# Kernel tuning notes

Hardware: AMD Instinct MI355X
Metric: run time of the kernel (lower is better)

## Reference

```python
import jax, jax.numpy as jnp
import numpy as np
from functools import reduce

N_QUBITS = 12          # input_shape[-2] = 2**12 = 4096; must be multiple of 4
DIM = 2 ** N_QUBITS
N_GATES = N_QUBITS // 4  # one diamond U-gate (4 qubits, 16x16) per group
BATCH = 128
TWO_PI = 6.283185307179586


def setup_inputs() -> dict:
    key = jax.random.key(0)
    k1, k2, k3, k4 = jax.random.split(key, 4)
    thetas = jax.random.uniform(k1, (N_GATES,), jnp.float32, 0.0, TWO_PI)
    # Fixed Hermitian generator for the 16x16 gate, pre-diagonalized:
    # U(theta) = V @ diag(exp(-i*theta*evals)) @ V^T
    rng = np.random.RandomState(42)
    H = rng.randn(16, 16).astype(np.float32)
    H = (H + H.T) * 0.5
    evals_np, evecs_np = np.linalg.eigh(H)
    evecs = jnp.asarray(evecs_np, jnp.float32)
    evals = jnp.asarray(evals_np, jnp.float32)
    state_real = jax.random.normal(k3, (BATCH, DIM, 1), jnp.float32)
    state_imag = jax.random.normal(k4, (BATCH, DIM, 1), jnp.float32)
    return {"thetas": thetas, "evecs": evecs, "evals": evals,
            "state_real": state_real, "state_imag": state_imag}


def _gate(theta, evecs, evals):
    # 16x16 unitary: V diag(exp(-i theta lambda)) V^T  (V real orthogonal)
    phase = jnp.exp(-1j * (theta * evals).astype(jnp.complex64))  # [16]
    V = evecs.astype(jnp.complex64)
    return (V * phase[None, :]) @ V.T  # [16,16] complex64


def reference(thetas, evecs, evals, state_real, state_imag):
    # Build each 4-qubit gate, then the full unitary via Kronecker product
    Us = [_gate(thetas[i], evecs, evals) for i in range(N_GATES)]
    U_full = reduce(jnp.kron, Us)  # [DIM, DIM] complex64 (the anti-pattern)
    psi = state_real.astype(jnp.complex64) + 1j * state_imag.astype(jnp.complex64)
    out = jnp.einsum('ij,bjk->bik', U_full, psi)  # U @ inputs
    # stack real/imag so output is a single real array: [2, BATCH, DIM, 1]
    return jnp.stack([jnp.real(out), jnp.imag(out)])
```

## Files before the change

kernel.cpp:

```cpp
#include <hip/hip_runtime.h>

#define DIM 4096
#define NB 128
#define S1 17
#define S0 274

__global__ __launch_bounds__(256)
void ulayer_kernel(const float* __restrict__ thetas,
                   const float* __restrict__ evecs,
                   const float* __restrict__ evals,
                   const float* __restrict__ sre,
                   const float* __restrict__ sim,
                   float* __restrict__ out)
{
    __shared__ float  sV[256];
    __shared__ float  sC[48];
    __shared__ float  sS[48];
    __shared__ float2 sG[3][16][16];
    __shared__ float2 st[16 * S0];

    const int t = threadIdx.x;
    const int b = blockIdx.x;

    sV[t] = evecs[t];
    if (t < 48) {
        const int g = t >> 4, k = t & 15;
        const float a = thetas[g] * evals[k];
        float sn, cs;
        sincosf(a, &sn, &cs);
        sC[t] = cs;
        sS[t] = sn;
    }

    const float4* __restrict__ vre = (const float4*)(sre + (size_t)b * DIM);
    const float4* __restrict__ vim = (const float4*)(sim + (size_t)b * DIM);
    float4 lre[4], lim[4];
#pragma unroll
    for (int it = 0; it < 4; ++it) {
        lre[it] = vre[t + 256 * it];
        lim[it] = vim[t + 256 * it];
    }

    __syncthreads();

#pragma unroll
    for (int rep = 0; rep < 3; ++rep) {
        const int e = t + (rep << 8);
        const int g = e >> 8;
        const int i = (e >> 4) & 15;
        const int j = e & 15;
        float gr = 0.f, gi = 0.f;
#pragma unroll
        for (int k = 0; k < 16; ++k) {
            const float vv = sV[i * 16 + k] * sV[j * 16 + k];
            gr = fmaf(vv,  sC[(g << 4) + k], gr);
            gi = fmaf(vv, -sS[(g << 4) + k], gi);
        }
        sG[g][i][j] = make_float2(gr, gi);
    }

#pragma unroll
    for (int it = 0; it < 4; ++it) {
        const int e0 = (t + 256 * it) << 2;
        const int i0 = e0 >> 8;
        const int r  = e0 & 255;
        const int base = i0 * S0 + (r >> 4) * S1 + (r & 15);
        const float* pr = (const float*)&lre[it];
        const float* pi = (const float*)&lim[it];
#pragma unroll
        for (int q = 0; q < 4; ++q)
            st[base + q] = make_float2(pr[q], pi[q]);
    }
    __syncthreads();

    const int h = t >> 4;
    const int k = t & 15;

    auto pass = [&](const int gidx, const int base, const int stride) {
        float2 x[16];
#pragma unroll
        for (int j = 0; j < 16; ++j) x[j] = st[base + j * stride];
        float2 y[16];
#pragma unroll
        for (int i = 0; i < 16; ++i) {
            float ar = 0.f, ai = 0.f;
#pragma unroll
            for (int j = 0; j < 16; ++j) {
                const float2 g = sG[gidx][i][j];
                ar = fmaf(g.x,  x[j].x, ar);
                ar = fmaf(-g.y, x[j].y, ar);
                ai = fmaf(g.x,  x[j].y, ai);
                ai = fmaf(g.y,  x[j].x, ai);
            }
            y[i] = make_float2(ar, ai);
        }
#pragma unroll
        for (int i = 0; i < 16; ++i) st[base + i * stride] = y[i];
    };

    pass(2, h * S0 + k * S1, 1);
    __syncthreads();
    pass(1, h * S0 + k, S1);
    __syncthreads();
    pass(0, h * S1 + k, S0);
    __syncthreads();

    float* __restrict__ ore = out + (size_t)b * DIM;
    float* __restrict__ oim = out + (size_t)NB * DIM + (size_t)b * DIM;
#pragma unroll
    for (int it = 0; it < 4; ++it) {
        const int e0 = (t + 256 * it) << 2;
        const int i0 = e0 >> 8;
        const int r  = e0 & 255;
        const int base = i0 * S0 + (r >> 4) * S1 + (r & 15);
        float4 xr, xi;
        float* qr = (float*)&xr;
        float* qi = (float*)&xi;
#pragma unroll
        for (int q = 0; q < 4; ++q) {
            const float2 v = st[base + q];
            qr[q] = v.x;
            qi[q] = v.y;
        }
        *(float4*)(ore + e0) = xr;
        *(float4*)(oim + e0) = xi;
    }
}

extern "C" void kernel_launch(void* const* d_in, const int* in_sizes, int n_in,
                              void* d_out, int out_size, void* d_ws, size_t ws_size,
                              hipStream_t stream) {
    const float* thetas = (const float*)d_in[0];
    const float* evecs  = (const float*)d_in[1];
    const float* evals  = (const float*)d_in[2];
    const float* sre    = (const float*)d_in[3];
    const float* sim    = (const float*)d_in[4];
    float* out = (float*)d_out;
    ulayer_kernel<<<NB, 256, 0, stream>>>(thetas, evecs, evals, sre, sim, out);
}
```

Baseline: 78.91 us.

## Double threads per block and split gate rows across threads in each pass

Moves the block from 256 to 512 threads. Each thread now keeps two gate rows in registers and handles four fibers, where it previously handled one full 16-row fiber. Because a fiber's outputs are now written by several threads, each pass gets an extra barrier between reading inputs and writing results. The aim is more waves per CU to hide LDS latency while keeping per-thread register use in check, at the cost of reading each fiber's inputs 8x redundantly from LDS and adding barriers.

After: 70.16 us. 11.1% less time.

```diff
diff --git a/kernel.cpp b/kernel.cpp
--- a/kernel.cpp
+++ b/kernel.cpp
@@ -2,10 +2,11 @@
 
 #define DIM 4096
 #define NB 128
+#define NT 512
 #define S1 17
 #define S0 274
 
-__global__ __launch_bounds__(256)
+__global__ __launch_bounds__(NT)
 void ulayer_kernel(const float* __restrict__ thetas,
                    const float* __restrict__ evecs,
                    const float* __restrict__ evals,
@@ -22,46 +23,48 @@
     const int t = threadIdx.x;
     const int b = blockIdx.x;
 
-    sV[t] = evecs[t];
-    if (t < 48) {
-        const int g = t >> 4, k = t & 15;
-        const float a = thetas[g] * evals[k];
+    if (t < 256) sV[t] = evecs[t];
+    else if (t < 304) {
+        const int e = t - 256;
+        const int g = e >> 4, k = e & 15;
         float sn, cs;
-        sincosf(a, &sn, &cs);
-        sC[t] = cs;
-        sS[t] = sn;
+        sincosf(thetas[g] * evals[k], &sn, &cs);
+        sC[e] = cs;
+        sS[e] = sn;
     }
 
     const float4* __restrict__ vre = (const float4*)(sre + (size_t)b * DIM);
     const float4* __restrict__ vim = (const float4*)(sim + (size_t)b * DIM);
-    float4 lre[4], lim[4];
+    float4 lre[2], lim[2];
 #pragma unroll
-    for (int it = 0; it < 4; ++it) {
-        lre[it] = vre[t + 256 * it];
-        lim[it] = vim[t + 256 * it];
+    for (int it = 0; it < 2; ++it) {
+        lre[it] = vre[t + NT * it];
+        lim[it] = vim[t + NT * it];
     }
 
     __syncthreads();
 
 #pragma unroll
-    for (int rep = 0; rep < 3; ++rep) {
-        const int e = t + (rep << 8);
-        const int g = e >> 8;
-        const int i = (e >> 4) & 15;
-        const int j = e & 15;
-        float gr = 0.f, gi = 0.f;
+    for (int rep = 0; rep < 2; ++rep) {
+        const int e = t + (rep << 9);
+        if (e < 768) {
+            const int g = e >> 8;
+            const int i = (e >> 4) & 15;
+            const int j = e & 15;
+            float gr = 0.f, gi = 0.f;
 #pragma unroll
-        for (int k = 0; k < 16; ++k) {
-            const float vv = sV[i * 16 + k] * sV[j * 16 + k];
-            gr = fmaf(vv,  sC[(g << 4) + k], gr);
-            gi = fmaf(vv, -sS[(g << 4) + k], gi);
+            for (int k = 0; k < 16; ++k) {
+                const float vv = sV[i * 16 + k] * sV[j * 16 + k];
+                gr = fmaf(vv,  sC[(g << 4) + k], gr);
+                gi = fmaf(vv, -sS[(g << 4) + k], gi);
+            }
+            sG[g][i][j] = make_float2(gr, gi);
         }
-        sG[g][i][j] = make_float2(gr, gi);
     }
 
 #pragma unroll
-    for (int it = 0; it < 4; ++it) {
-        const int e0 = (t + 256 * it) << 2;
+    for (int it = 0; it < 2; ++it) {
+        const int e0 = (t + NT * it) << 2;
         const int i0 = e0 >> 8;
         const int r  = e0 & 255;
         const int base = i0 * S0 + (r >> 4) * S1 + (r & 15);
@@ -73,43 +76,64 @@
     }
     __syncthreads();
 
-    const int h = t >> 4;
-    const int k = t & 15;
+    const int fg = t & 63;
+    const int ih = t >> 6;
+    const int r0 = ih * 2;
 
-    auto pass = [&](const int gidx, const int base, const int stride) {
-        float2 x[16];
+    auto pass = [&](const int gidx, const int BH, const int BK, const int STRIDE) {
+        float2 g0[16], g1[16];
 #pragma unroll
-        for (int j = 0; j < 16; ++j) x[j] = st[base + j * stride];
-        float2 y[16];
+        for (int j = 0; j < 16; ++j) {
+            g0[j] = sG[gidx][r0][j];
+            g1[j] = sG[gidx][r0 + 1][j];
+        }
+        float2 y0[4], y1[4];
 #pragma unroll
-        for (int i = 0; i < 16; ++i) {
-            float ar = 0.f, ai = 0.f;
+        for (int fl = 0; fl < 4; ++fl) {
+            const int f = fg + 64 * fl;
+            const int h = f >> 4;
+            const int k = f & 15;
+            const int base = h * BH + k * BK;
+            float2 x[16];
+#pragma unroll
+            for (int j = 0; j < 16; ++j) x[j] = st[base + j * STRIDE];
+            float ar0 = 0.f, ai0 = 0.f, ar1 = 0.f, ai1 = 0.f;
 #pragma unroll
             for (int j = 0; j < 16; ++j) {
-                const float2 g = sG[gidx][i][j];
-                ar = fmaf(g.x,  x[j].x, ar);
-                ar = fmaf(-g.y, x[j].y, ar);
-                ai = fmaf(g.x,  x[j].y, ai);
-                ai = fmaf(g.y,  x[j].x, ai);
+                ar0 = fmaf(g0[j].x,  x[j].x, ar0);
+                ar0 = fmaf(-g0[j].y, x[j].y, ar0);
+                ai0 = fmaf(g0[j].x,  x[j].y, ai0);
+                ai0 = fmaf(g0[j].y,  x[j].x, ai0);
+                ar1 = fmaf(g1[j].x,  x[j].x, ar1);
+                ar1 = fmaf(-g1[j].y, x[j].y, ar1);
+                ai1 = fmaf(g1[j].x,  x[j].y, ai1);
+                ai1 = fmaf(g1[j].y,  x[j].x, ai1);
             }
-            y[i] = make_float2(ar, ai);
+            y0[fl] = make_float2(ar0, ai0);
+            y1[fl] = make_float2(ar1, ai1);
         }
+        __syncthreads();
 #pragma unroll
-        for (int i = 0; i < 16; ++i) st[base + i * stride] = y[i];
+        for (int fl = 0; fl < 4; ++fl) {
+            const int f = fg + 64 * fl;
+            const int h = f >> 4;
+            const int k = f & 15;
+            const int base = h * BH + k * BK;
+            st[base + r0 * STRIDE]       = y0[fl];
+            st[base + (r0 + 1) * STRIDE] = y1[fl];
+        }
+        __syncthreads();
     };
 
-    pass(2, h * S0 + k * S1, 1);
-    __syncthreads();
-    pass(1, h * S0 + k, S1);
-    __syncthreads();
-    pass(0, h * S1 + k, S0);
-    __syncthreads();
+    pass(2, S0, S1, 1);
+    pass(1, S0, 1, S1);
+    pass(0, S1, 1, S0);
 
     float* __restrict__ ore = out + (size_t)b * DIM;
     float* __restrict__ oim = out + (size_t)NB * DIM + (size_t)b * DIM;
 #pragma unroll
-    for (int it = 0; it < 4; ++it) {
-        const int e0 = (t + 256 * it) << 2;
+    for (int it = 0; it < 2; ++it) {
+        const int e0 = (t + NT * it) << 2;
         const int i0 = e0 >> 8;
         const int r  = e0 & 255;
         const int base = i0 * S0 + (r >> 4) * S1 + (r & 15);
@@ -136,5 +160,5 @@
     const float* sre    = (const float*)d_in[3];
     const float* sim    = (const float*)d_in[4];
     float* out = (float*)d_out;
-    ulayer_kernel<<<NB, 256, 0, stream>>>(thetas, evecs, evals, sre, sim, out);
+    ulayer_kernel<<<NB, NT, 0, stream>>>(thetas, evecs, evals, sre, sim, out);
 }
```

## Split contraction into two kernels with four blocks per batch row

Applied to the files above, without the earlier changes.

Replaces the single 128-block kernel with two kernels of 512 blocks each. The first applies gates 2 and 1 on quarter-slices of each state and writes the intermediate complex state to workspace. The second applies gate 0 across the remaining axis. The contraction pass is also restructured so each thread holds two gate rows in registers rather than reading the gate from shared memory. This targets low occupancy, since only 128 blocks were spread over the GPU, at the cost of an extra launch, a global round trip for the intermediate state, and recomputing the gates in every block.

Result: faster. 73.70 us (-6.6%).

```diff
diff --git a/kernel.cpp b/kernel.cpp
--- a/kernel.cpp
+++ b/kernel.cpp
@@ -1,52 +1,95 @@
 #include <hip/hip_runtime.h>
 
 #define DIM 4096
-#define NB 128
-#define S1 17
-#define S0 274
+#define BATCH 128
+#define K1S0 274
+#define K1S1 17
+#define K2S0 69
+#define K2S1 17
+
+__device__ __forceinline__ void contract_pass(float2* __restrict__ st,
+                                              const float2 (*__restrict__ G)[16],
+                                              const int t, const int BH,
+                                              const int BK, const int STRIDE)
+{
+    const int fpair = t & 31;
+    const int r0 = (t >> 5) << 1;
+    float2 g0[16], g1[16];
+#pragma unroll
+    for (int j = 0; j < 16; ++j) {
+        g0[j] = G[r0][j];
+        g1[j] = G[r0 + 1][j];
+    }
+    float2 y[2][2];
+#pragma unroll
+    for (int fl = 0; fl < 2; ++fl) {
+        const int f = fpair + (fl << 5);
+        const int base = (f >> 4) * BH + (f & 15) * BK;
+        float2 x[16];
+#pragma unroll
+        for (int j = 0; j < 16; ++j) x[j] = st[base + j * STRIDE];
+        float ar0 = 0.f, ai0 = 0.f, ar1 = 0.f, ai1 = 0.f;
+#pragma unroll
+        for (int j = 0; j < 16; ++j) {
+            ar0 = fmaf(g0[j].x,  x[j].x, ar0);
+            ar0 = fmaf(-g0[j].y, x[j].y, ar0);
+            ai0 = fmaf(g0[j].x,  x[j].y, ai0);
+            ai0 = fmaf(g0[j].y,  x[j].x, ai0);
+            ar1 = fmaf(g1[j].x,  x[j].x, ar1);
+            ar1 = fmaf(-g1[j].y, x[j].y, ar1);
+            ai1 = fmaf(g1[j].x,  x[j].y, ai1);
+            ai1 = fmaf(g1[j].y,  x[j].x, ai1);
+        }
+        y[fl][0] = make_float2(ar0, ai0);
+        y[fl][1] = make_float2(ar1, ai1);
+    }
+    __syncthreads();
+#pragma unroll
+    for (int fl = 0; fl < 2; ++fl) {
+        const int f = fpair + (fl << 5);
+        const int base = (f >> 4) * BH + (f & 15) * BK;
+        st[base + r0 * STRIDE]       = y[fl][0];
+        st[base + (r0 + 1) * STRIDE] = y[fl][1];
+    }
+    __syncthreads();
+}
 
 __global__ __launch_bounds__(256)
-void ulayer_kernel(const float* __restrict__ thetas,
-                   const float* __restrict__ evecs,
-                   const float* __restrict__ evals,
-                   const float* __restrict__ sre,
-                   const float* __restrict__ sim,
-                   float* __restrict__ out)
+void ulayer_k1(const float* __restrict__ thetas,
+               const float* __restrict__ evecs,
+               const float* __restrict__ evals,
+               const float* __restrict__ sre,
+               const float* __restrict__ sim,
+               float2* __restrict__ ws)
 {
     __shared__ float  sV[256];
     __shared__ float  sC[48];
     __shared__ float  sS[48];
     __shared__ float2 sG[3][16][16];
-    __shared__ float2 st[16 * S0];
+    __shared__ float2 st[4 * K1S0];
 
     const int t = threadIdx.x;
-    const int b = blockIdx.x;
+    const int b = blockIdx.x >> 2;
+    const int q = blockIdx.x & 3;
 
     sV[t] = evecs[t];
     if (t < 48) {
         const int g = t >> 4, k = t & 15;
-        const float a = thetas[g] * evals[k];
         float sn, cs;
-        sincosf(a, &sn, &cs);
+        sincosf(thetas[g] * evals[k], &sn, &cs);
         sC[t] = cs;
         sS[t] = sn;
     }
 
-    const float4* __restrict__ vre = (const float4*)(sre + (size_t)b * DIM);
-    const float4* __restrict__ vim = (const float4*)(sim + (size_t)b * DIM);
-    float4 lre[4], lim[4];
-#pragma unroll
-    for (int it = 0; it < 4; ++it) {
-        lre[it] = vre[t + 256 * it];
-        lim[it] = vim[t + 256 * it];
-    }
-
-    __syncthreads();
-
-#pragma unroll
-    for (int rep = 0; rep < 3; ++rep) {
+    const float4 re4 = *(const float4*)(sre + (size_t)b * DIM + q * 1024 + t * 4);
+    const float4 im4 = *(const float4*)(sim + (size_t)b * DIM + q * 1024 + t * 4);
+
+    __syncthreads();
+
+#pragma unroll
+    for (int rep = 0; rep < 2; ++rep) {
         const int e = t + (rep << 8);
-        const int g = e >> 8;
+        const int g = 1 + (e >> 8);
         const int i = (e >> 4) & 15;
         const int j = e & 15;
         float gr = 0.f, gi = 0.f;
@@ -59,72 +102,93 @@
         sG[g][i][j] = make_float2(gr, gi);
     }
 
-#pragma unroll
-    for (int it = 0; it < 4; ++it) {
-        const int e0 = (t + 256 * it) << 2;
-        const int i0 = e0 >> 8;
-        const int r  = e0 & 255;
-        const int base = i0 * S0 + (r >> 4) * S1 + (r & 15);
-        const float* pr = (const float*)&lre[it];
-        const float* pi = (const float*)&lim[it];
-#pragma unroll
-        for (int q = 0; q < 4; ++q)
-            st[base + q] = make_float2(pr[q], pi[q]);
-    }
-    __syncthreads();
-
-    const int h = t >> 4;
-    const int k = t & 15;
-
-    auto pass = [&](const int gidx, const int base, const int stride) {
-        float2 x[16];
-#pragma unroll
-        for (int j = 0; j < 16; ++j) x[j] = st[base + j * stride];
-        float2 y[16];
-#pragma unroll
-        for (int i = 0; i < 16; ++i) {
-            float ar = 0.f, ai = 0.f;
-#pragma unroll
-            for (int j = 0; j < 16; ++j) {
-                const float2 g = sG[gidx][i][j];
-                ar = fmaf(g.x,  x[j].x, ar);
-                ar = fmaf(-g.y, x[j].y, ar);
-                ai = fmaf(g.x,  x[j].y, ai);
-                ai = fmaf(g.y,  x[j].x, ai);
-            }
-            y[i] = make_float2(ar, ai);
+    const int e0  = t << 2;
+    const int li0 = e0 >> 8;
+    const int i1  = (e0 >> 4) & 15;
+    const int i2  = e0 & 15;
+    const int sbase = li0 * K1S0 + i1 * K1S1 + i2;
+    st[sbase + 0] = make_float2(re4.x, im4.x);
+    st[sbase + 1] = make_float2(re4.y, im4.y);
+    st[sbase + 2] = make_float2(re4.z, im4.z);
+    st[sbase + 3] = make_float2(re4.w, im4.w);
+    __syncthreads();
+
+    contract_pass(st, sG[2], t, K1S0, K1S1, 1);
+    contract_pass(st, sG[1], t, K1S0, 1, K1S1);
+
+    const float2 a0 = st[sbase + 0];
+    const float2 a1 = st[sbase + 1];
+    const float2 a2 = st[sbase + 2];
+    const float2 a3 = st[sbase + 3];
+    float4* wp = (float4*)(ws + (size_t)b * DIM + q * 1024 + e0);
+    wp[0] = make_float4(a0.x, a0.y, a1.x, a1.y);
+    wp[1] = make_float4(a2.x, a2.y, a3.x, a3.y);
+}
+
+__global__ __launch_bounds__(256)
+void ulayer_k2(const float* __restrict__ thetas,
+               const float* __restrict__ evecs,
+               const float* __restrict__ evals,
+               const float2* __restrict__ ws,
+               float* __restrict__ out)
+{
+    __shared__ float  sV[256];
+    __shared__ float  sC[16];
+    __shared__ float  sS[16];
+    __shared__ float2 sG0[16][16];
+    __shared__ float2 st[16 * K2S0];
+
+    const int t = threadIdx.x;
+    const int b = blockIdx.x >> 2;
+    const int p = blockIdx.x & 3;
+
+    sV[t] = evecs[t];
+    if (t < 16) {
+        float sn, cs;
+        sincosf(thetas[0] * evals[t], &sn, &cs);
+        sC[t] = cs;
+        sS[t] = sn;
+    }
+
+    const int i0 = t >> 4;
+    const int r0 = (t & 15) << 2;
+    const float2* wrow = ws + (size_t)b * DIM + i0 * 256 + p * 64 + r0;
+    const float4 w0 = *(const float4*)(wrow);
+    const float4 w1 = *(const float4*)(wrow + 2);
+
+    __syncthreads();
+
+    {
+        const int i = t >> 4;
+        const int j = t & 15;
+        float gr = 0.f, gi = 0.f;
+#pragma unroll
+        for (int k = 0; k < 16; ++k) {
+            const float vv = sV[i * 16 + k] * sV[j * 16 + k];
+            gr = fmaf(vv,  sC[k], gr);
+            gi = fmaf(vv, -sS[k], gi);
         }
-#pragma unroll
-        for (int i = 0; i < 16; ++i) st[base + i * stride] = y[i];
-    };
-
-    pass(2, h * S0 + k * S1, 1);
-    __syncthreads();
-    pass(1, h * S0 + k, S1);
-    __syncthreads();
-    pass(0, h * S1 + k, S0);
-    __syncthreads();
-
-    float* __restrict__ ore = out + (size_t)b * DIM;
-    float* __restrict__ oim = out + (size_t)NB * DIM + (size_t)b * DIM;
-#pragma unroll
-    for (int it = 0; it < 4; ++it) {
-        const int e0 = (t + 256 * it) << 2;
-        const int i0 = e0 >> 8;
-        const int r  = e0 & 255;
-        const int base = i0 * S0 + (r >> 4) * S1 + (r & 15);
-        float4 xr, xi;
-        float* qr = (float*)&xr;
-        float* qi = (float*)&xi;
-#pragma unroll
-        for (int q = 0; q < 4; ++q) {
-            const float2 v = st[base + q];
-            qr[q] = v.x;
-            qi[q] = v.y;
-        }
-        *(float4*)(ore + e0) = xr;
-        *(float4*)(oim + e0) = xi;
-    }
+        sG0[i][j] = make_float2(gr, gi);
+    }
+
+    const int li1 = r0 >> 4;
+    const int i2  = r0 & 15;
+    const int sbase = i0 * K2S0 + li1 * K2S1 + i2;
+    st[sbase + 0] = make_float2(w0.x, w0.y);
+    st[sbase + 1] = make_float2(w0.z, w0.w);
+    st[sbase + 2] = make_float2(w1.x, w1.y);
+    st[sbase + 3] = make_float2(w1.z, w1.w);
+    __syncthreads();
+
+    contract_pass(st, sG0, t, K2S1, 1, K2S0);
+
+    const float2 a0 = st[sbase + 0];
+    const float2 a1 = st[sbase + 1];
+    const float2 a2 = st[sbase + 2];
+    const float2 a3 = st[sbase + 3];
+    const size_t ooff = (size_t)b * DIM + i0 * 256 + p * 64 + r0;
+    *(float4*)(out + ooff) = make_float4(a0.x, a1.x, a2.x, a3.x);
+    *(float4*)(out + (size_t)BATCH * DIM + ooff) = make_float4(a0.y, a1.y, a2.y, a3.y);
 }
 
 extern "C" void kernel_launch(void* const* d_in, const int* in_sizes, int n_in,
@@ -136,5 +200,8 @@
     const float* sre    = (const float*)d_in[3];
     const float* sim    = (const float*)d_in[4];
     float* out = (float*)d_out;
-    ulayer_kernel<<<NB, 256, 0, stream>>>(thetas, evecs, evals, sre, sim, out);
-}
+    float2* ws = (float2*)d_ws;
+
+    ulayer_k1<<<BATCH * 4, 256, 0, stream>>>(thetas, evecs, evals, sre, sim, ws);
+    ulayer_k2<<<BATCH * 4, 256, 0, stream>>>(thetas, evecs, evals, ws, out);
+}
```

## Use 1024 threads per block with row-split gate passes and fused output

Applied to the files above, without the earlier changes.

Raises the block size from 256 to 1024 threads. Each thread now computes two output rows for two fibers, holding its gate rows in registers, instead of one thread doing a full 16x16 matvec per fiber. The last pass writes results straight to global memory, which removes the final shared-memory readback. The cost is an extra barrier inside each pass and scalar, less coalesced global stores, while more waves per CU are meant to hide latency.

Result: faster. 71.07 us (-9.9%).

```diff
diff --git a/kernel.cpp b/kernel.cpp
--- a/kernel.cpp
+++ b/kernel.cpp
@@ -1,11 +1,12 @@
 #include <hip/hip_runtime.h>
 
 #define DIM 4096
-#define NB 128
+#define BATCH 128
+#define NT 1024
 #define S1 17
 #define S0 274
 
-__global__ __launch_bounds__(256)
+__global__ __launch_bounds__(NT)
 void ulayer_kernel(const float* __restrict__ thetas,
                    const float* __restrict__ evecs,
                    const float* __restrict__ evals,
@@ -22,33 +23,24 @@
     const int t = threadIdx.x;
     const int b = blockIdx.x;
 
-    sV[t] = evecs[t];
-    if (t < 48) {
-        const int g = t >> 4, k = t & 15;
-        const float a = thetas[g] * evals[k];
+    if (t < 256) sV[t] = evecs[t];
+    else if (t < 304) {
+        const int e = t - 256;
         float sn, cs;
-        sincosf(a, &sn, &cs);
-        sC[t] = cs;
-        sS[t] = sn;
+        sincosf(thetas[e >> 4] * evals[e & 15], &sn, &cs);
+        sC[e] = cs;
+        sS[e] = sn;
     }
 
-    const float4* __restrict__ vre = (const float4*)(sre + (size_t)b * DIM);
-    const float4* __restrict__ vim = (const float4*)(sim + (size_t)b * DIM);
-    float4 lre[4], lim[4];
-#pragma unroll
-    for (int it = 0; it < 4; ++it) {
-        lre[it] = vre[t + 256 * it];
-        lim[it] = vim[t + 256 * it];
-    }
+    const float4 re4 = *(const float4*)(sre + (size_t)b * DIM + (t << 2));
+    const float4 im4 = *(const float4*)(sim + (size_t)b * DIM + (t << 2));
 
     __syncthreads();
 
-#pragma unroll
-    for (int rep = 0; rep < 3; ++rep) {
-        const int e = t + (rep << 8);
-        const int g = e >> 8;
-        const int i = (e >> 4) & 15;
-        const int j = e & 15;
+    if (t < 768) {
+        const int g = t >> 8;
+        const int i = (t >> 4) & 15;
+        const int j = t & 15;
         float gr = 0.f, gi = 0.f;
 #pragma unroll
         for (int k = 0; k < 16; ++k) {
@@ -59,71 +51,91 @@
         sG[g][i][j] = make_float2(gr, gi);
     }
 
-#pragma unroll
-    for (int it = 0; it < 4; ++it) {
-        const int e0 = (t + 256 * it) << 2;
-        const int i0 = e0 >> 8;
-        const int r  = e0 & 255;
-        const int base = i0 * S0 + (r >> 4) * S1 + (r & 15);
-        const float* pr = (const float*)&lre[it];
-        const float* pi = (const float*)&lim[it];
-#pragma unroll
-        for (int q = 0; q < 4; ++q)
-            st[base + q] = make_float2(pr[q], pi[q]);
-    }
+    const int e0 = t << 2;
+    const int sbase = (e0 >> 8) * S0 + ((e0 >> 4) & 15) * S1 + (e0 & 15);
+    st[sbase + 0] = make_float2(re4.x, im4.x);
+    st[sbase + 1] = make_float2(re4.y, im4.y);
+    st[sbase + 2] = make_float2(re4.z, im4.z);
+    st[sbase + 3] = make_float2(re4.w, im4.w);
     __syncthreads();
 
-    const int h = t >> 4;
-    const int k = t & 15;
+    const int fg = t & 127;
+    const int r0 = (t >> 7) << 1;
 
-    auto pass = [&](const int gidx, const int base, const int stride) {
-        float2 x[16];
+    auto pass = [&](const float2 (*__restrict__ G)[16],
+                    const int BH, const int BK, const int STRIDE) {
+        float2 g0[16], g1[16];
 #pragma unroll
-        for (int j = 0; j < 16; ++j) x[j] = st[base + j * stride];
-        float2 y[16];
+        for (int j = 0; j < 16; ++j) {
+            g0[j] = G[r0][j];
+            g1[j] = G[r0 + 1][j];
+        }
+        float2 y[2][2];
 #pragma unroll
-        for (int i = 0; i < 16; ++i) {
-            float ar = 0.f, ai = 0.f;
+        for (int fl = 0; fl < 2; ++fl) {
+            const int f = fg + (fl << 7);
+            const int base = (f >> 4) * BH + (f & 15) * BK;
+            float ar0 = 0.f, ai0 = 0.f, ar1 = 0.f, ai1 = 0.f;
 #pragma unroll
             for (int j = 0; j < 16; ++j) {
-                const float2 g = sG[gidx][i][j];
-                ar = fmaf(g.x,  x[j].x, ar);
-                ar = fmaf(-g.y, x[j].y, ar);
-                ai = fmaf(g.x,  x[j].y, ai);
-                ai = fmaf(g.y,  x[j].x, ai);
+                const float2 x = st[base + j * STRIDE];
+                ar0 = fmaf(g0[j].x,  x.x, ar0);
+                ar0 = fmaf(-g0[j].y, x.y, ar0);
+                ai0 = fmaf(g0[j].x,  x.y, ai0);
+                ai0 = fmaf(g0[j].y,  x.x, ai0);
+                ar1 = fmaf(g1[j].x,  x.x, ar1);
+                ar1 = fmaf(-g1[j].y, x.y, ar1);
+                ai1 = fmaf(g1[j].x,  x.y, ai1);
+                ai1 = fmaf(g1[j].y,  x.x, ai1);
             }
-            y[i] = make_float2(ar, ai);
+            y[fl][0] = make_float2(ar0, ai0);
+            y[fl][1] = make_float2(ar1, ai1);
         }
+        __syncthreads();
 #pragma unroll
-        for (int i = 0; i < 16; ++i) st[base + i * stride] = y[i];
+        for (int fl = 0; fl < 2; ++fl) {
+            const int f = fg + (fl << 7);
+            const int base = (f >> 4) * BH + (f & 15) * BK;
+            st[base + r0 * STRIDE]       = y[fl][0];
+            st[base + (r0 + 1) * STRIDE] = y[fl][1];
+        }
+        __syncthreads();
     };
 
-    pass(2, h * S0 + k * S1, 1);
-    __syncthreads();
-    pass(1, h * S0 + k, S1);
-    __syncthreads();
-    pass(0, h * S1 + k, S0);
-    __syncthreads();
+    pass(sG[2], S0, S1, 1);
+    pass(sG[1], S0, 1, S1);
 
-    float* __restrict__ ore = out + (size_t)b * DIM;
-    float* __restrict__ oim = out + (size_t)NB * DIM + (size_t)b * DIM;
+    {
+        float2 g0[16], g1[16];
 #pragma unroll
-    for (int it = 0; it < 4; ++it) {
-        const int e0 = (t + 256 * it) << 2;
-        const int i0 = e0 >> 8;
-        const int r  = e0 & 255;
-        const int base = i0 * S0 + (r >> 4) * S1 + (r & 15);
-        float4 xr, xi;
-        float* qr = (float*)&xr;
-        float* qi = (float*)&xi;
+        for (int j = 0; j < 16; ++j) {
+            g0[j] = sG[0][r0][j];
+            g1[j] = sG[0][r0 + 1][j];
+        }
+        float* __restrict__ ore = out + (size_t)b * DIM;
+        float* __restrict__ oim = out + (size_t)BATCH * DIM + (size_t)b * DIM;
 #pragma unroll
-        for (int q = 0; q < 4; ++q) {
-            const float2 v = st[base + q];
-            qr[q] = v.x;
-            qi[q] = v.y;
+        for (int fl = 0; fl < 2; ++fl) {
+            const int f = fg + (fl << 7);
+            const int base = (f >> 4) * S1 + (f & 15);
+            float ar0 = 0.f, ai0 = 0.f, ar1 = 0.f, ai1 = 0.f;
+#pragma unroll
+            for (int j = 0; j < 16; ++j) {
+                const float2 x = st[base + j * S0];
+                ar0 = fmaf(g0[j].x,  x.x, ar0);
+                ar0 = fmaf(-g0[j].y, x.y, ar0);
+                ai0 = fmaf(g0[j].x,  x.y, ai0);
+                ai0 = fmaf(g0[j].y,  x.x, ai0);
+                ar1 = fmaf(g1[j].x,  x.x, ar1);
+                ar1 = fmaf(-g1[j].y, x.y, ar1);
+                ai1 = fmaf(g1[j].x,  x.y, ai1);
+                ai1 = fmaf(g1[j].y,  x.x, ai1);
+            }
+            ore[r0 * 256 + f]       = ar0;
+            oim[r0 * 256 + f]       = ai0;
+            ore[(r0 + 1) * 256 + f] = ar1;
+            oim[(r0 + 1) * 256 + f] = ai1;
         }
-        *(float4*)(ore + e0) = xr;
-        *(float4*)(oim + e0) = xi;
     }
 }
 
@@ -136,5 +148,5 @@
     const float* sre    = (const float*)d_in[3];
     const float* sim    = (const float*)d_in[4];
     float* out = (float*)d_out;
-    ulayer_kernel<<<NB, 256, 0, stream>>>(thetas, evecs, evals, sre, sim, out);
+    ulayer_kernel<<<BATCH, NT, 0, stream>>>(thetas, evecs, evals, sre, sim, out);
 }
```
